# Kernel tuning notes

Hardware: AMD Instinct MI355X
Metric: run time of the kernel (lower is better)

The kernel has to match this reference:

```python
import jax, jax.numpy as jnp
import numpy as np

DIM = 384
HEADS = 8
HEAD_DIM = DIM // HEADS
TEM_LEN = 400
SCALE = HEAD_DIM ** -0.5


def setup_inputs() -> dict:
    key = jax.random.key(0)
    ks = jax.random.split(key, 12)
    B, Lq, Lkv = 16, 1024, 1424
    inp = {
        'tem_mask': jax.random.normal(ks[0], (B, TEM_LEN, DIM), jnp.float32),
        'search_mask': jax.random.normal(ks[1], (B, Lkv - TEM_LEN, DIM), jnp.float32),
        'q': jax.random.normal(ks[2], (B, Lq, DIM), jnp.float32),
        'kv': jax.random.normal(ks[3], (B, Lkv, DIM), jnp.float32),
        'attn_pos': jax.random.normal(ks[4], (1, HEADS, Lq, Lkv), jnp.float32),
        # learned params (attn_pos_encoding_only=True: q, fused kv, proj)
        'q_w': jax.random.normal(ks[5], (DIM, DIM), jnp.float32) * 0.02,
        'q_b': jnp.zeros((DIM,), jnp.float32),
        'kv_w': jax.random.normal(ks[6], (2 * DIM, DIM), jnp.float32) * 0.02,
        'kv_b': jnp.zeros((2 * DIM,), jnp.float32),
        'proj_w': jax.random.normal(ks[7], (DIM, DIM), jnp.float32) * 0.02,
        'proj_b': jnp.zeros((DIM,), jnp.float32),
    }
    return inp


def reference(tem_mask, search_mask, q, kv, attn_pos, q_w, q_b, kv_w, kv_b, proj_w, proj_b):
    B, Lq, C = q.shape
    Lkv = kv.shape[1]
    # projections
    qh = (q @ q_w.T + q_b).reshape(B, Lq, HEADS, HEAD_DIM).transpose(0, 2, 1, 3)  # (B,H,Lq,hd)
    kvp = kv @ kv_w.T + kv_b                                                      # (B,Lkv,2C)
    k = kvp[..., :C]
    v = kvp[..., C:]
    # additive masks on v before head split (template tokens first, then search)
    v = jnp.concatenate([v[:, :TEM_LEN] + tem_mask, v[:, TEM_LEN:] + search_mask], axis=1)
    kh = k.reshape(B, Lkv, HEADS, HEAD_DIM).transpose(0, 2, 1, 3)  # (B,H,Lkv,hd)
    vh = v.reshape(B, Lkv, HEADS, HEAD_DIM).transpose(0, 2, 1, 3)  # (B,H,Lkv,hd)
    # scaled scores + untied positional bias, softmax over keys
    attn = jnp.einsum('bhqd,bhkd->bhqk', qh, kh) * SCALE + attn_pos
    attn = jax.nn.softmax(attn, axis=-1)
    x = jnp.einsum('bhqk,bhkd->bhqd', attn, vh)
    x = x.transpose(0, 2, 1, 3).reshape(B, Lq, C)
    return x @ proj_w.T + proj_b
```

## Files before the change

kernel.cpp:

```cpp
#include <hip/hip_runtime.h>
#include <stdint.h>

#define NB 16
#define NH 8
#define LQ 1024
#define LKV 1424
#define LKVP 1472
#define DIMC 384
#define NKVT 23
#define TEM 400
#define QSCALE 0.20823509f
#define LOG2E_F 1.4426950408889634f

typedef __attribute__((ext_vector_type(4))) float f32x4;
typedef __attribute__((ext_vector_type(8))) short bf16x8;
typedef __attribute__((ext_vector_type(4))) unsigned short us4;
typedef __attribute__((ext_vector_type(2))) unsigned int u32x2;
typedef __attribute__((ext_vector_type(4))) unsigned int u32x4;

__device__ __forceinline__ unsigned short f2b(float f) {
  unsigned int u = __builtin_bit_cast(unsigned int, f);
  u += 0x7fffu + ((u >> 16) & 1u);
  return (unsigned short)(u >> 16);
}
__device__ __forceinline__ float b2f(unsigned short u) {
  return __builtin_bit_cast(float, (unsigned int)u << 16);
}

__device__ __forceinline__ void gload_lds16(const void* gsrc, void* ldst) {
  __builtin_amdgcn_global_load_lds(
      (const __attribute__((address_space(1))) void*)gsrc,
      (__attribute__((address_space(3))) void*)ldst, 16, 0, 0);
}

__global__ __launch_bounds__(256) void conv_swz(const float* __restrict__ in,
                                                unsigned short* __restrict__ out, int nch) {
  int i = blockIdx.x * 256 + threadIdx.x;
  if (i >= nch) return;
  int row = i / 48, ch = i - row * 48;
  const float* src = in + (size_t)row * DIMC + ch * 8;
  f32x4 x = *(const f32x4*)src;
  f32x4 y = *(const f32x4*)(src + 4);
  bf16x8 o;
  o[0] = (short)f2b(x[0]); o[1] = (short)f2b(x[1]);
  o[2] = (short)f2b(x[2]); o[3] = (short)f2b(x[3]);
  o[4] = (short)f2b(y[0]); o[5] = (short)f2b(y[1]);
  o[6] = (short)f2b(y[2]); o[7] = (short)f2b(y[3]);
  int blk = ch >> 3, c3 = (ch & 7) ^ (row & 7);
  *(bf16x8*)(out + (size_t)row * DIMC + blk * 64 + c3 * 8) = o;
}

__global__ __launch_bounds__(256) void zero_qpad(unsigned short* Qp) {
  int r = blockIdx.x * 256 + threadIdx.x;
  u32x4 z = {0u, 0u, 0u, 0u};
  *(u32x4*)(Qp + (size_t)r * 64 + 48) = z;
  *(u32x4*)(Qp + (size_t)r * 64 + 56) = z;
}
__global__ __launch_bounds__(256) void zero_kpad(unsigned short* Kp) {
  int r = blockIdx.x * 256 + threadIdx.x;
  int s = r % LKVP;
  unsigned short* row = Kp + (size_t)r * 64;
  u32x4 z = {0u, 0u, 0u, 0u};
  if (s < LKV) {
    *(u32x4*)(row + (6 ^ (s & 7)) * 8) = z;
    *(u32x4*)(row + (7 ^ (s & 7)) * 8) = z;
  } else {
#pragma unroll
    for (int c = 0; c < 64; c += 8) *(u32x4*)(row + c) = z;
  }
}
__global__ __launch_bounds__(256) void zero_vpad(unsigned short* Vt) {
  int i = blockIdx.x * 256 + threadIdx.x;
  int row = i / 6, x = 2 + i - (i / 6) * 6;
  int d = row % 48;
  u32x4 z = {0u, 0u, 0u, 0u};
  *(u32x4*)(Vt + (size_t)row * LKVP + 1408 + ((x ^ d) & 7) * 8) = z;
}

__global__ __launch_bounds__(256) void prep_pos(const float* __restrict__ pos,
                                                unsigned short* __restrict__ posb) {
  const int t = blockIdx.x, h = blockIdx.z;
  const int wave = threadIdx.x >> 6, lane = threadIdx.x & 63;
  const int q16 = blockIdx.y * 4 + wave;
  const int l16 = lane & 15, g = lane >> 4;
  const int q = q16 * 16 + l16;
  const float* pr = pos + ((size_t)h * LQ + q) * LKV;
  unsigned short vals[16];
  const unsigned short NEG = f2b(-1e30f);
#pragma unroll
  for (int ni = 0; ni < 4; ++ni) {
    if (t * 64 + ni * 16 < LKV) {
      f32x4 v = *(const f32x4*)(pr + t * 64 + ni * 16 + 4 * g);
#pragma unroll
      for (int r = 0; r < 4; ++r) vals[ni * 4 + r] = f2b(v[r] * LOG2E_F);
    } else {
#pragma unroll
      for (int r = 0; r < 4; ++r) vals[ni * 4 + r] = NEG;
    }
  }
  unsigned short* op = posb + ((((size_t)h * 64 + q16) * NKVT + t) * 64 + lane) * 16;
  bf16x8 a, b;
#pragma unroll
  for (int i = 0; i < 8; ++i) { a[i] = (short)vals[i]; b[i] = (short)vals[8 + i]; }
  *(bf16x8*)op = a;
  *(bf16x8*)(op + 8) = b;
}

template <int MODE>
__global__ __launch_bounds__(256) void proj_gemm(
    const unsigned short* __restrict__ A, const unsigned short* __restrict__ Wb,
    const float* __restrict__ bias, const float* __restrict__ tem,
    const float* __restrict__ srch, unsigned short* __restrict__ Oq,
    unsigned short* __restrict__ Ok, unsigned short* __restrict__ Ovt,
    float* __restrict__ Of) {
  __shared__ unsigned short Ash[128 * 64];
  __shared__ unsigned short Bsh[128 * 64];
  const int tid = threadIdx.x;
  const int lane = tid & 63, l16 = lane & 15, g = lane >> 4;
  const int wave = tid >> 6, wm = wave >> 1, wn = wave & 1;
  const int n0 = blockIdx.x * 128, m0 = blockIdx.y * 128;

  f32x4 acc[4][4];
#pragma unroll
  for (int i = 0; i < 4; ++i)
#pragma unroll
    for (int j = 0; j < 4; ++j) { f32x4 z = {0.f, 0.f, 0.f, 0.f}; acc[i][j] = z; }

  const char* Abase = (const char*)A + (size_t)m0 * 768;
  const char* Bbase = (const char*)Wb + (size_t)n0 * 768;

  for (int ks = 0; ks < 6; ++ks) {
    __syncthreads();
#pragma unroll
    for (int rnd = 0; rnd < 4; ++rnd) {
      int idx = tid + rnd * 256;
      int row = idx >> 3, chunk = idx & 7;
      gload_lds16(Abase + (size_t)row * 768 + ks * 128 + chunk * 16,
                  (char*)Ash + idx * 16);
    }
#pragma unroll
    for (int rnd = 0; rnd < 4; ++rnd) {
      int idx = tid + rnd * 256;
      int row = idx >> 3, chunk = idx & 7;
      gload_lds16(Bbase + (size_t)row * 768 + ks * 128 + chunk * 16,
                  (char*)Bsh + idx * 16);
    }
    asm volatile("s_waitcnt vmcnt(0)" ::: "memory");
    __syncthreads();
#pragma unroll
    for (int kk = 0; kk < 2; ++kk) {
      bf16x8 a[4], bb[4];
#pragma unroll
      for (int mi = 0; mi < 4; ++mi) {
        int row = wm * 64 + mi * 16 + l16;
        a[mi] = *(const bf16x8*)((char*)Ash + row * 128 + (((g + 4 * kk) ^ (row & 7)) << 4));
      }
#pragma unroll
      for (int ni = 0; ni < 4; ++ni) {
        int row = wn * 64 + ni * 16 + l16;
        bb[ni] = *(const bf16x8*)((char*)Bsh + row * 128 + (((g + 4 * kk) ^ (row & 7)) << 4));
      }
#pragma unroll
      for (int mi = 0; mi < 4; ++mi)
#pragma unroll
        for (int ni = 0; ni < 4; ++ni)
          acc[mi][ni] = __builtin_amdgcn_mfma_f32_16x16x32_bf16(a[mi], bb[ni], acc[mi][ni], 0, 0, 0);
    }
  }

#pragma unroll
  for (int mi = 0; mi < 4; ++mi) {
    const int m_g0 = m0 + wm * 64 + mi * 16 + 4 * g;
#pragma unroll
    for (int ni = 0; ni < 4; ++ni) {
      const int n_g = n0 + wn * 64 + ni * 16 + l16;
      const float bv = bias[n_g];
      if (MODE == 0) {
        const int hh = n_g / 48, d = n_g - hh * 48;
#pragma unroll
        for (int r = 0; r < 4; ++r) {
          const int m_g = m_g0 + r;
          const int b = m_g >> 10, m = m_g & 1023;
          Oq[(((size_t)b * NH + hh) * LQ + m) * 64 + d] = f2b((acc[mi][ni][r] + bv) * QSCALE);
        }
      } else if (MODE == 2) {
#pragma unroll
        for (int r = 0; r < 4; ++r)
          Of[(size_t)(m_g0 + r) * DIMC + n_g] = acc[mi][ni][r] + bv;
      } else {
        const int b = m_g0 / LKV, s0 = m_g0 - b * LKV;
        if (n_g < DIMC) {
          const int hh = n_g / 48, d = n_g - hh * 48;
#pragma unroll
          for (int r = 0; r < 4; ++r) {
            const int s = s0 + r;
            const int dsw = (d & 7) | ((((d >> 3) ^ (s & 7)) & 7) << 3);
            Ok[(((size_t)b * NH + hh) * LKVP + s) * 64 + dsw] = f2b(acc[mi][ni][r] + bv);
          }
        } else {
          const int c = n_g - DIMC, hh = c / 48, d = c - hh * 48;
          const float* mb = (s0 < TEM)
                                ? tem + ((size_t)b * TEM + s0) * DIMC + c
                                : srch + ((size_t)b * (LKV - TEM) + (s0 - TEM)) * DIMC + c;
          const int off = s0 & 63;
          const int soff = (s0 & ~63) | ((((off >> 3) ^ d) & 7) << 3) | (off & 7);
          us4 pk;
#pragma unroll
          for (int r = 0; r < 4; ++r)
            pk[r] = f2b(acc[mi][ni][r] + bv + mb[(size_t)r * DIMC]);
          *(us4*)(Ovt + (((size_t)b * NH + hh) * 48 + d) * LKVP + soff) = pk;
        }
      }
    }
  }
}

__device__ __forceinline__ void stage_tile(const char* kbase, const char* vbase, int t,
                                           char* kdst, char* vdst, int wave, int lane) {
  const char* ks = kbase + (size_t)t * 8192 + wave * 2048 + lane * 16;
  char* kd = kdst + wave * 2048;
  gload_lds16(ks, kd);
  gload_lds16(ks + 1024, kd + 1024);
  if (wave < 3) {
    const char* vs = vbase + (size_t)(wave * 16 + (lane >> 3)) * (LKVP * 2) +
                     (size_t)t * 128 + (lane & 7) * 16;
    char* vd = vdst + wave * 2048;
    gload_lds16(vs, vd);
    gload_lds16(vs + 8 * (LKVP * 2), vd + 1024);
  }
}

__global__ __launch_bounds__(256, 4) void attn_fwd(
    const unsigned short* __restrict__ posb, const unsigned short* __restrict__ Qp,
    const unsigned short* __restrict__ Kp, const unsigned short* __restrict__ Vt,
    unsigned short* __restrict__ X) {
  __shared__ unsigned short Ksh[2][64 * 64];
  __shared__ unsigned short Vsh[2][48 * 64];
  __shared__ unsigned short Psh[4][16 * 64];

  const int tid = threadIdx.x;
  const int lane = tid & 63, l16 = lane & 15, g = lane >> 4;
  const int wave = tid >> 6;
  const int bid = blockIdx.x;
  const int bh = bid & 127, qt = bid >> 7;
  const int b = bh >> 3, h = bh & 7;
  const int qrow = qt * 128 + wave * 32;

  bf16x8 qf[2][2];
#pragma unroll
  for (int qs = 0; qs < 2; ++qs) {
    const unsigned short* qb = Qp + ((size_t)bh * LQ + qrow + qs * 16 + l16) * 64 + 8 * g;
    qf[qs][0] = *(const bf16x8*)qb;
    qf[qs][1] = *(const bf16x8*)(qb + 32);
  }

  float m_run[2] = {-1e30f, -1e30f}, l_run[2] = {0.f, 0.f};
  f32x4 o[2][3];
#pragma unroll
  for (int qs = 0; qs < 2; ++qs)
#pragma unroll
    for (int d = 0; d < 3; ++d) { f32x4 z = {0.f, 0.f, 0.f, 0.f}; o[qs][d] = z; }

  const char* kbase = (const char*)(Kp + (size_t)bh * LKVP * 64);
  const char* vbase = (const char*)(Vt + (size_t)bh * 48 * LKVP);
  const int q16b = qt * 8 + wave * 2;
  const unsigned short* pq0 = posb + (((size_t)h * 64 + q16b) * NKVT) * 1024 + lane * 16;
  const unsigned short* pq1 = pq0 + (size_t)NKVT * 1024;
  char* pbase = (char*)&Psh[wave][0] + l16 * 128;
  const int swz = (l16 & 7) << 4;

  stage_tile(kbase, vbase, 0, (char*)&Ksh[0][0], (char*)&Vsh[0][0], wave, lane);
  asm volatile("s_waitcnt vmcnt(0)" ::: "memory");
  __syncthreads();

  int buf = 0;
  for (int t = 0; t < NKVT; ++t) {
    if (t + 1 < NKVT)
      stage_tile(kbase, vbase, t + 1, (char*)&Ksh[buf ^ 1][0], (char*)&Vsh[buf ^ 1][0],
                 wave, lane);

    bf16x8 pA0 = *(const bf16x8*)(pq0);
    bf16x8 pA1 = *(const bf16x8*)(pq0 + 8);
    bf16x8 pB0 = *(const bf16x8*)(pq1);
    bf16x8 pB1 = *(const bf16x8*)(pq1 + 8);
    pq0 += 1024; pq1 += 1024;

    f32x4 s[2][4];
#pragma unroll
    for (int qs = 0; qs < 2; ++qs)
#pragma unroll
      for (int ni = 0; ni < 4; ++ni) { f32x4 z = {0.f, 0.f, 0.f, 0.f}; s[qs][ni] = z; }
#pragma unroll
    for (int ni = 0; ni < 4; ++ni) {
      const int krow = ni * 16 + l16;
      const char* kr = (const char*)&Ksh[buf][0] + krow * 128;
      bf16x8 kf0 = *(const bf16x8*)(kr + ((g ^ (krow & 7)) << 4));
      bf16x8 kf1 = *(const bf16x8*)(kr + (((g + 4) ^ (krow & 7)) << 4));
      s[0][ni] = __builtin_amdgcn_mfma_f32_16x16x32_bf16(kf0, qf[0][0], s[0][ni], 0, 0, 0);
      s[0][ni] = __builtin_amdgcn_mfma_f32_16x16x32_bf16(kf1, qf[0][1], s[0][ni], 0, 0, 0);
      s[1][ni] = __builtin_amdgcn_mfma_f32_16x16x32_bf16(kf0, qf[1][0], s[1][ni], 0, 0, 0);
      s[1][ni] = __builtin_amdgcn_mfma_f32_16x16x32_bf16(kf1, qf[1][1], s[1][ni], 0, 0, 0);
    }

    bf16x8 af[2][2];
#pragma unroll
    for (int qs = 0; qs < 2; ++qs) {
      float x[16];
#pragma unroll
      for (int ni = 0; ni < 4; ++ni)
#pragma unroll
        for (int r = 0; r < 4; ++r) {
          const int idx = ni * 4 + r;
          unsigned short u =
              (unsigned short)(qs == 0 ? (idx < 8 ? pA0[idx] : pA1[idx - 8])
                                       : (idx < 8 ? pB0[idx] : pB1[idx - 8]));
          x[idx] = s[qs][ni][r] + b2f(u);
        }
      float mx = x[0];
#pragma unroll
      for (int i = 1; i < 16; ++i) mx = fmaxf(mx, x[i]);
      mx = fmaxf(mx, __shfl_xor(mx, 16));
      mx = fmaxf(mx, __shfl_xor(mx, 32));
      if (__any(mx > m_run[qs] + 8.f)) {
        const float mn = fmaxf(m_run[qs], mx);
        const float al = exp2f(m_run[qs] - mn);
        m_run[qs] = mn;
        l_run[qs] *= al;
#pragma unroll
        for (int r = 0; r < 4; ++r) {
          const float ab = __shfl(al, 4 * (lane >> 4) + r);
          o[qs][0][r] *= ab; o[qs][1][r] *= ab; o[qs][2][r] *= ab;
        }
      }
      const float base = m_run[qs];
      float sum = 0.f;
#pragma unroll
      for (int i = 0; i < 16; ++i) { x[i] = exp2f(x[i] - base); sum += x[i]; }
      sum += __shfl_xor(sum, 16);
      sum += __shfl_xor(sum, 32);
      l_run[qs] += sum;

#pragma unroll
      for (int ni = 0; ni < 4; ++ni) {
        unsigned int lo, hi;
        asm("v_cvt_pk_bf16_f32 %0, %1, %2" : "=v"(lo) : "v"(x[4 * ni]), "v"(x[4 * ni + 1]));
        asm("v_cvt_pk_bf16_f32 %0, %1, %2" : "=v"(hi) : "v"(x[4 * ni + 2]), "v"(x[4 * ni + 3]));
        u32x2 pk = {lo, hi};
        *(u32x2*)(pbase + ((32 * ni + 8 * g) ^ swz)) = pk;
      }
      af[qs][0] = *(const bf16x8*)(pbase + ((16 * g) ^ swz));
      af[qs][1] = *(const bf16x8*)(pbase + ((64 + 16 * g) ^ swz));
    }

#pragma unroll
    for (int dn = 0; dn < 3; ++dn) {
      const int vr = 16 * dn + l16;
      const char* vrp = (const char*)&Vsh[buf][0] + vr * 128;
      bf16x8 vf0 = *(const bf16x8*)(vrp + ((g ^ (vr & 7)) << 4));
      bf16x8 vf1 = *(const bf16x8*)(vrp + (((g + 4) ^ (vr & 7)) << 4));
      o[0][dn] = __builtin_amdgcn_mfma_f32_16x16x32_bf16(af[0][0], vf0, o[0][dn], 0, 0, 0);
      o[0][dn] = __builtin_amdgcn_mfma_f32_16x16x32_bf16(af[0][1], vf1, o[0][dn], 0, 0, 0);
      o[1][dn] = __builtin_amdgcn_mfma_f32_16x16x32_bf16(af[1][0], vf0, o[1][dn], 0, 0, 0);
      o[1][dn] = __builtin_amdgcn_mfma_f32_16x16x32_bf16(af[1][1], vf1, o[1][dn], 0, 0, 0);
    }

    asm volatile("s_waitcnt vmcnt(0)" ::: "memory");
    __syncthreads();
    buf ^= 1;
  }

#pragma unroll
  for (int qs = 0; qs < 2; ++qs) {
    const float linv = 1.f / l_run[qs];
#pragma unroll
    for (int r = 0; r < 4; ++r) {
      const float ib = __shfl(linv, 4 * (lane >> 4) + r);
      const int m = qrow + qs * 16 + 4 * g + r;
#pragma unroll
      for (int dn = 0; dn < 3; ++dn) {
        const int c = h * 48 + 16 * dn + l16;
        const int cs = (c & ~63) | (c & 7) | ((((c >> 3) & 7) ^ (m & 7)) << 3);
        X[((size_t)b * LQ + m) * DIMC + cs] = f2b(o[qs][dn][r] * ib);
      }
    }
  }
}

extern "C" void kernel_launch(void* const* d_in, const int* in_sizes, int n_in,
                              void* d_out, int out_size, void* d_ws, size_t ws_size,
                              hipStream_t stream) {
  const float* tem  = (const float*)d_in[0];
  const float* srch = (const float*)d_in[1];
  const float* q    = (const float*)d_in[2];
  const float* kv   = (const float*)d_in[3];
  const float* pos  = (const float*)d_in[4];
  const float* q_w  = (const float*)d_in[5];
  const float* q_b  = (const float*)d_in[6];
  const float* kv_w = (const float*)d_in[7];
  const float* kv_b = (const float*)d_in[8];
  const float* p_w  = (const float*)d_in[9];
  const float* p_b  = (const float*)d_in[10];
  float* out = (float*)d_out;

  char* w = (char*)d_ws;
  unsigned short* Qp   = (unsigned short*)(w);
  unsigned short* Kp   = (unsigned short*)(w + 16777216);
  unsigned short* Vt   = (unsigned short*)(w + 40894464);
  unsigned short* X    = (unsigned short*)(w + 58982400);
  unsigned short* qb   = X;
  unsigned short* posb = (unsigned short*)(w + 71565312);
  unsigned short* kvb  = (unsigned short*)(w + 95682560);
  unsigned short* qwb  = (unsigned short*)(w + 113180672);
  unsigned short* kvwb = (unsigned short*)(w + 113475584);
  unsigned short* pwb  = (unsigned short*)(w + 114065408);

  conv_swz<<<3072, 256, 0, stream>>>(q, qb, 16384 * 48);
  conv_swz<<<4272, 256, 0, stream>>>(kv, kvb, 22784 * 48);
  conv_swz<<<72, 256, 0, stream>>>(q_w, qwb, 384 * 48);
  conv_swz<<<144, 256, 0, stream>>>(kv_w, kvwb, 768 * 48);
  conv_swz<<<72, 256, 0, stream>>>(p_w, pwb, 384 * 48);
  zero_qpad<<<512, 256, 0, stream>>>(Qp);
  zero_kpad<<<736, 256, 0, stream>>>(Kp);
  zero_vpad<<<144, 256, 0, stream>>>(Vt);
  prep_pos<<<dim3(NKVT, 16, NH), 256, 0, stream>>>(pos, posb);
  proj_gemm<0><<<dim3(3, 128), 256, 0, stream>>>(qb, qwb, q_b, nullptr, nullptr,
                                                 Qp, nullptr, nullptr, nullptr);
  proj_gemm<1><<<dim3(6, 178), 256, 0, stream>>>(kvb, kvwb, kv_b, tem, srch,
                                                 nullptr, Kp, Vt, nullptr);
  attn_fwd<<<1024, 256, 0, stream>>>(posb, Qp, Kp, Vt, X);
  proj_gemm<2><<<dim3(3, 128), 256, 0, stream>>>(X, pwb, p_b, nullptr, nullptr,
                                                 nullptr, nullptr, nullptr, out);
}
```

Before: 233.0 us.

## Merge prep launches, coalesce pos prep via LDS, restructure attention softmax/PV

Merges the five conversion launches into one kernel and the three pad-zeroing launches into another, cutting launch count. prep_pos now reads contiguous 64-wide rows coalesced and transposes through shared memory before writing the bf16 layout, fixing strided global reads. In attention, the positional bias is preloaded directly as the score accumulator init (saving adds), and softmax/pack/PV for the two query subtiles are interleaved so MFMA on one overlaps VALU work on the other. This adds branching in the merged kernels and extra LDS use in prep_pos.

```diff
diff --git a/kernel.cpp b/kernel.cpp
--- a/kernel.cpp
+++ b/kernel.cpp
@@ -23,9 +23,6 @@
   u += 0x7fffu + ((u >> 16) & 1u);
   return (unsigned short)(u >> 16);
 }
-__device__ __forceinline__ float b2f(unsigned short u) {
-  return __builtin_bit_cast(float, (unsigned int)u << 16);
-}
 
 __device__ __forceinline__ void gload_lds16(const void* gsrc, void* ldst) {
   __builtin_amdgcn_global_load_lds(
@@ -33,77 +30,97 @@
       (__attribute__((address_space(3))) void*)ldst, 16, 0, 0);
 }
 
-__global__ __launch_bounds__(256) void conv_swz(const float* __restrict__ in,
-                                                unsigned short* __restrict__ out, int nch) {
+__global__ __launch_bounds__(256) void conv_all(
+    const float* __restrict__ q, const float* __restrict__ kv,
+    const float* __restrict__ qw, const float* __restrict__ kvw,
+    const float* __restrict__ pw, unsigned short* __restrict__ qb,
+    unsigned short* __restrict__ kvb, unsigned short* __restrict__ qwb,
+    unsigned short* __restrict__ kvwb, unsigned short* __restrict__ pwb) {
   int i = blockIdx.x * 256 + threadIdx.x;
-  if (i >= nch) return;
+  const float* src;
+  unsigned short* dst;
+  if (i < 16384 * 48) { src = q; dst = qb; }
+  else if (i < 39168 * 48) { i -= 16384 * 48; src = kv; dst = kvb; }
+  else if (i < 39552 * 48) { i -= 39168 * 48; src = qw; dst = qwb; }
+  else if (i < 40320 * 48) { i -= 39552 * 48; src = kvw; dst = kvwb; }
+  else if (i < 40704 * 48) { i -= 40320 * 48; src = pw; dst = pwb; }
+  else return;
   int row = i / 48, ch = i - row * 48;
-  const float* src = in + (size_t)row * DIMC + ch * 8;
-  f32x4 x = *(const f32x4*)src;
-  f32x4 y = *(const f32x4*)(src + 4);
+  const float* sp = src + (size_t)row * DIMC + ch * 8;
+  f32x4 x = *(const f32x4*)sp;
+  f32x4 y = *(const f32x4*)(sp + 4);
   bf16x8 o;
   o[0] = (short)f2b(x[0]); o[1] = (short)f2b(x[1]);
   o[2] = (short)f2b(x[2]); o[3] = (short)f2b(x[3]);
   o[4] = (short)f2b(y[0]); o[5] = (short)f2b(y[1]);
   o[6] = (short)f2b(y[2]); o[7] = (short)f2b(y[3]);
   int blk = ch >> 3, c3 = (ch & 7) ^ (row & 7);
-  *(bf16x8*)(out + (size_t)row * DIMC + blk * 64 + c3 * 8) = o;
-}
-
-__global__ __launch_bounds__(256) void zero_qpad(unsigned short* Qp) {
-  int r = blockIdx.x * 256 + threadIdx.x;
+  *(bf16x8*)(dst + (size_t)row * DIMC + blk * 64 + c3 * 8) = o;
+}
+
+__global__ __launch_bounds__(256) void zero_pads(unsigned short* Qp, unsigned short* Kp,
+                                                 unsigned short* Vt) {
+  int i = blockIdx.x * 256 + threadIdx.x;
   u32x4 z = {0u, 0u, 0u, 0u};
-  *(u32x4*)(Qp + (size_t)r * 64 + 48) = z;
-  *(u32x4*)(Qp + (size_t)r * 64 + 56) = z;
-}
-__global__ __launch_bounds__(256) void zero_kpad(unsigned short* Kp) {
-  int r = blockIdx.x * 256 + threadIdx.x;
-  int s = r % LKVP;
-  unsigned short* row = Kp + (size_t)r * 64;
-  u32x4 z = {0u, 0u, 0u, 0u};
-  if (s < LKV) {
-    *(u32x4*)(row + (6 ^ (s & 7)) * 8) = z;
-    *(u32x4*)(row + (7 ^ (s & 7)) * 8) = z;
-  } else {
-#pragma unroll
-    for (int c = 0; c < 64; c += 8) *(u32x4*)(row + c) = z;
-  }
-}
-__global__ __launch_bounds__(256) void zero_vpad(unsigned short* Vt) {
-  int i = blockIdx.x * 256 + threadIdx.x;
-  int row = i / 6, x = 2 + i - (i / 6) * 6;
-  int d = row % 48;
-  u32x4 z = {0u, 0u, 0u, 0u};
-  *(u32x4*)(Vt + (size_t)row * LKVP + 1408 + ((x ^ d) & 7) * 8) = z;
+  if (i < 131072) {
+    *(u32x4*)(Qp + (size_t)i * 64 + 48) = z;
+    *(u32x4*)(Qp + (size_t)i * 64 + 56) = z;
+  } else if (i < 131072 + 188416) {
+    int r = i - 131072;
+    int s = r % LKVP;
+    unsigned short* row = Kp + (size_t)r * 64;
+    if (s < LKV) {
+      *(u32x4*)(row + (6 ^ (s & 7)) * 8) = z;
+      *(u32x4*)(row + (7 ^ (s & 7)) * 8) = z;
+    } else {
+#pragma unroll
+      for (int c = 0; c < 64; c += 8) *(u32x4*)(row + c) = z;
+    }
+  } else if (i < 131072 + 188416 + 36864) {
+    int j = i - 319488;
+    int row = j / 6, x = 2 + j - (j / 6) * 6;
+    int d = row % 48;
+    *(u32x4*)(Vt + (size_t)row * LKVP + 1408 + ((x ^ d) & 7) * 8) = z;
+  }
 }
 
 __global__ __launch_bounds__(256) void prep_pos(const float* __restrict__ pos,
                                                 unsigned short* __restrict__ posb) {
-  const int t = blockIdx.x, h = blockIdx.z;
+  __shared__ float lds[4][1024];
   const int wave = threadIdx.x >> 6, lane = threadIdx.x & 63;
-  const int q16 = blockIdx.y * 4 + wave;
   const int l16 = lane & 15, g = lane >> 4;
-  const int q = q16 * 16 + l16;
-  const float* pr = pos + ((size_t)h * LQ + q) * LKV;
-  unsigned short vals[16];
-  const unsigned short NEG = f2b(-1e30f);
-#pragma unroll
-  for (int ni = 0; ni < 4; ++ni) {
-    if (t * 64 + ni * 16 < LKV) {
-      f32x4 v = *(const f32x4*)(pr + t * 64 + ni * 16 + 4 * g);
-#pragma unroll
-      for (int r = 0; r < 4; ++r) vals[ni * 4 + r] = f2b(v[r] * LOG2E_F);
-    } else {
-#pragma unroll
-      for (int r = 0; r < 4; ++r) vals[ni * 4 + r] = NEG;
-    }
-  }
-  unsigned short* op = posb + ((((size_t)h * 64 + q16) * NKVT + t) * 64 + lane) * 16;
-  bf16x8 a, b;
-#pragma unroll
-  for (int i = 0; i < 8; ++i) { a[i] = (short)vals[i]; b[i] = (short)vals[8 + i]; }
-  *(bf16x8*)op = a;
-  *(bf16x8*)(op + 8) = b;
+  const int q16 = blockIdx.x, h = blockIdx.y;
+  float* L = &lds[wave][0];
+
+  for (int t = wave; t < NKVT; t += 4) {
+#pragma unroll
+    for (int i = 0; i < 4; ++i) {
+      const int row = i * 4 + g;
+      const int gcol = t * 64 + l16 * 4;
+      f32x4 v;
+      if (gcol < LKV) {
+        v = *(const f32x4*)(pos + ((size_t)h * LQ + q16 * 16 + row) * LKV + gcol);
+        v *= LOG2E_F;
+      } else {
+        f32x4 neg = {-1e30f, -1e30f, -1e30f, -1e30f};
+        v = neg;
+      }
+      *(f32x4*)(L + row * 64 + ((l16 ^ (row & 7)) << 2)) = v;
+    }
+    unsigned short vals[16];
+#pragma unroll
+    for (int ni = 0; ni < 4; ++ni) {
+      f32x4 wv = *(const f32x4*)(L + l16 * 64 + (((4 * ni + g) ^ (l16 & 7)) << 2));
+#pragma unroll
+      for (int r = 0; r < 4; ++r) vals[4 * ni + r] = f2b(wv[r]);
+    }
+    unsigned short* op = posb + ((((size_t)h * 64 + q16) * NKVT + t) * 64 + lane) * 16;
+    bf16x8 a, b;
+#pragma unroll
+    for (int k = 0; k < 8; ++k) { a[k] = (short)vals[k]; b[k] = (short)vals[8 + k]; }
+    *(bf16x8*)op = a;
+    *(bf16x8*)(op + 8) = b;
+  }
 }
 
 template <int MODE>
@@ -230,6 +247,57 @@
   }
 }
 
+__device__ __forceinline__ void softmax16(f32x4 (&sx)[4], float& m_run, float& l_run,
+                                          f32x4& o0, f32x4& o1, f32x4& o2, int lane) {
+  float a0 = fmaxf(fmaxf(sx[0][0], sx[0][1]), sx[0][2]);
+  float a1 = fmaxf(fmaxf(sx[0][3], sx[1][0]), sx[1][1]);
+  float a2 = fmaxf(fmaxf(sx[1][2], sx[1][3]), sx[2][0]);
+  float a3 = fmaxf(fmaxf(sx[2][1], sx[2][2]), sx[2][3]);
+  float a4 = fmaxf(fmaxf(sx[3][0], sx[3][1]), sx[3][2]);
+  float mx = fmaxf(fmaxf(fmaxf(a0, a1), fmaxf(a2, a3)), fmaxf(a4, sx[3][3]));
+  mx = fmaxf(mx, __shfl_xor(mx, 16));
+  mx = fmaxf(mx, __shfl_xor(mx, 32));
+  if (__any(mx > m_run + 8.f)) {
+    const float mn = fmaxf(m_run, mx);
+    const float al = exp2f(m_run - mn);
+    m_run = mn;
+    l_run *= al;
+#pragma unroll
+    for (int r = 0; r < 4; ++r) {
+      const float ab = __shfl(al, 4 * (lane >> 4) + r);
+      o0[r] *= ab; o1[r] *= ab; o2[r] *= ab;
+    }
+  }
+  const float base = m_run;
+#pragma unroll
+  for (int ni = 0; ni < 4; ++ni)
+#pragma unroll
+    for (int r = 0; r < 4; ++r) sx[ni][r] = exp2f(sx[ni][r] - base);
+  float s0 = (sx[0][0] + sx[0][1]) + (sx[0][2] + sx[0][3]);
+  float s1 = (sx[1][0] + sx[1][1]) + (sx[1][2] + sx[1][3]);
+  float s2 = (sx[2][0] + sx[2][1]) + (sx[2][2] + sx[2][3]);
+  float s3 = (sx[3][0] + sx[3][1]) + (sx[3][2] + sx[3][3]);
+  float sum = (s0 + s1) + (s2 + s3);
+  sum += __shfl_xor(sum, 16);
+  sum += __shfl_xor(sum, 32);
+  l_run += sum;
+}
+
+__device__ __forceinline__ void packP(const f32x4 (&sx)[4], char* pbase, int swz, int g,
+                                      bf16x8& af0, bf16x8& af1) {
+#pragma unroll
+  for (int ni = 0; ni < 4; ++ni) {
+    float e0 = sx[ni][0], e1 = sx[ni][1], e2 = sx[ni][2], e3 = sx[ni][3];
+    unsigned int lo, hi;
+    asm("v_cvt_pk_bf16_f32 %0, %1, %2" : "=v"(lo) : "v"(e0), "v"(e1));
+    asm("v_cvt_pk_bf16_f32 %0, %1, %2" : "=v"(hi) : "v"(e2), "v"(e3));
+    u32x2 pk = {lo, hi};
+    *(u32x2*)(pbase + ((32 * ni + 8 * g) ^ swz)) = pk;
+  }
+  af0 = *(const bf16x8*)(pbase + ((16 * g) ^ swz));
+  af1 = *(const bf16x8*)(pbase + ((64 + 16 * g) ^ swz));
+}
+
 __global__ __launch_bounds__(256, 4) void attn_fwd(
     const unsigned short* __restrict__ posb, const unsigned short* __restrict__ Qp,
     const unsigned short* __restrict__ Kp, const unsigned short* __restrict__ Vt,
@@ -254,7 +322,7 @@
     qf[qs][1] = *(const bf16x8*)(qb + 32);
   }
 
-  float m_run[2] = {-1e30f, -1e30f}, l_run[2] = {0.f, 0.f};
+  float m_run0 = -1e30f, m_run1 = -1e30f, l_run0 = 0.f, l_run1 = 0.f;
   f32x4 o[2][3];
 #pragma unroll
   for (int qs = 0; qs < 2; ++qs)
@@ -279,89 +347,61 @@
       stage_tile(kbase, vbase, t + 1, (char*)&Ksh[buf ^ 1][0], (char*)&Vsh[buf ^ 1][0],
                  wave, lane);
 
-    bf16x8 pA0 = *(const bf16x8*)(pq0);
-    bf16x8 pA1 = *(const bf16x8*)(pq0 + 8);
-    bf16x8 pB0 = *(const bf16x8*)(pq1);
-    bf16x8 pB1 = *(const bf16x8*)(pq1 + 8);
+    u32x4 w0 = *(const u32x4*)(pq0);
+    u32x4 w1 = *(const u32x4*)(pq0 + 8);
+    u32x4 w2 = *(const u32x4*)(pq1);
+    u32x4 w3 = *(const u32x4*)(pq1 + 8);
     pq0 += 1024; pq1 += 1024;
 
-    f32x4 s[2][4];
-#pragma unroll
-    for (int qs = 0; qs < 2; ++qs)
-#pragma unroll
-      for (int ni = 0; ni < 4; ++ni) { f32x4 z = {0.f, 0.f, 0.f, 0.f}; s[qs][ni] = z; }
+    f32x4 s0[4], s1[4];
+#pragma unroll
+    for (int k = 0; k < 4; ++k) {
+      const int ni = k >> 1, j2 = (k & 1) * 2;
+      unsigned int a = w0[k], bb_ = w1[k], c = w2[k], d = w3[k];
+      s0[ni][j2]     = __builtin_bit_cast(float, a << 16);
+      s0[ni][j2 + 1] = __builtin_bit_cast(float, a & 0xffff0000u);
+      s0[ni + 2][j2]     = __builtin_bit_cast(float, bb_ << 16);
+      s0[ni + 2][j2 + 1] = __builtin_bit_cast(float, bb_ & 0xffff0000u);
+      s1[ni][j2]     = __builtin_bit_cast(float, c << 16);
+      s1[ni][j2 + 1] = __builtin_bit_cast(float, c & 0xffff0000u);
+      s1[ni + 2][j2]     = __builtin_bit_cast(float, d << 16);
+      s1[ni + 2][j2 + 1] = __builtin_bit_cast(float, d & 0xffff0000u);
+    }
+
 #pragma unroll
     for (int ni = 0; ni < 4; ++ni) {
       const int krow = ni * 16 + l16;
       const char* kr = (const char*)&Ksh[buf][0] + krow * 128;
       bf16x8 kf0 = *(const bf16x8*)(kr + ((g ^ (krow & 7)) << 4));
       bf16x8 kf1 = *(const bf16x8*)(kr + (((g + 4) ^ (krow & 7)) << 4));
-      s[0][ni] = __builtin_amdgcn_mfma_f32_16x16x32_bf16(kf0, qf[0][0], s[0][ni], 0, 0, 0);
-      s[0][ni] = __builtin_amdgcn_mfma_f32_16x16x32_bf16(kf1, qf[0][1], s[0][ni], 0, 0, 0);
-      s[1][ni] = __builtin_amdgcn_mfma_f32_16x16x32_bf16(kf0, qf[1][0], s[1][ni], 0, 0, 0);
-      s[1][ni] = __builtin_amdgcn_mfma_f32_16x16x32_bf16(kf1, qf[1][1], s[1][ni], 0, 0, 0);
-    }
-
-    bf16x8 af[2][2];
-#pragma unroll
-    for (int qs = 0; qs < 2; ++qs) {
-      float x[16];
-#pragma unroll
-      for (int ni = 0; ni < 4; ++ni)
-#pragma unroll
-        for (int r = 0; r < 4; ++r) {
-          const int idx = ni * 4 + r;
-          unsigned short u =
-              (unsigned short)(qs == 0 ? (idx < 8 ? pA0[idx] : pA1[idx - 8])
-                                       : (idx < 8 ? pB0[idx] : pB1[idx - 8]));
-          x[idx] = s[qs][ni][r] + b2f(u);
-        }
-      float mx = x[0];
-#pragma unroll
-      for (int i = 1; i < 16; ++i) mx = fmaxf(mx, x[i]);
-      mx = fmaxf(mx, __shfl_xor(mx, 16));
-      mx = fmaxf(mx, __shfl_xor(mx, 32));
-      if (__any(mx > m_run[qs] + 8.f)) {
-        const float mn = fmaxf(m_run[qs], mx);
-        const float al = exp2f(m_run[qs] - mn);
-        m_run[qs] = mn;
-        l_run[qs] *= al;
-#pragma unroll
-        for (int r = 0; r < 4; ++r) {
-          const float ab = __shfl(al, 4 * (lane >> 4) + r);
-          o[qs][0][r] *= ab; o[qs][1][r] *= ab; o[qs][2][r] *= ab;
-        }
-      }
-      const float base = m_run[qs];
-      float sum = 0.f;
-#pragma unroll
-      for (int i = 0; i < 16; ++i) { x[i] = exp2f(x[i] - base); sum += x[i]; }
-      sum += __shfl_xor(sum, 16);
-      sum += __shfl_xor(sum, 32);
-      l_run[qs] += sum;
-
-#pragma unroll
-      for (int ni = 0; ni < 4; ++ni) {
-        unsigned int lo, hi;
-        asm("v_cvt_pk_bf16_f32 %0, %1, %2" : "=v"(lo) : "v"(x[4 * ni]), "v"(x[4 * ni + 1]));
-        asm("v_cvt_pk_bf16_f32 %0, %1, %2" : "=v"(hi) : "v"(x[4 * ni + 2]), "v"(x[4 * ni + 3]));
-        u32x2 pk = {lo, hi};
-        *(u32x2*)(pbase + ((32 * ni + 8 * g) ^ swz)) = pk;
-      }
-      af[qs][0] = *(const bf16x8*)(pbase + ((16 * g) ^ swz));
-      af[qs][1] = *(const bf16x8*)(pbase + ((64 + 16 * g) ^ swz));
-    }
-
+      s0[ni] = __builtin_amdgcn_mfma_f32_16x16x32_bf16(kf0, qf[0][0], s0[ni], 0, 0, 0);
+      s0[ni] = __builtin_amdgcn_mfma_f32_16x16x32_bf16(kf1, qf[0][1], s0[ni], 0, 0, 0);
+      s1[ni] = __builtin_amdgcn_mfma_f32_16x16x32_bf16(kf0, qf[1][0], s1[ni], 0, 0, 0);
+      s1[ni] = __builtin_amdgcn_mfma_f32_16x16x32_bf16(kf1, qf[1][1], s1[ni], 0, 0, 0);
+    }
+
+    softmax16(s0, m_run0, l_run0, o[0][0], o[0][1], o[0][2], lane);
+    bf16x8 af00, af01, af10, af11;
+    packP(s0, pbase, swz, g, af00, af01);
+    softmax16(s1, m_run1, l_run1, o[1][0], o[1][1], o[1][2], lane);
 #pragma unroll
     for (int dn = 0; dn < 3; ++dn) {
       const int vr = 16 * dn + l16;
       const char* vrp = (const char*)&Vsh[buf][0] + vr * 128;
       bf16x8 vf0 = *(const bf16x8*)(vrp + ((g ^ (vr & 7)) << 4));
       bf16x8 vf1 = *(const bf16x8*)(vrp + (((g + 4) ^ (vr & 7)) << 4));
-      o[0][dn] = __builtin_amdgcn_mfma_f32_16x16x32_bf16(af[0][0], vf0, o[0][dn], 0, 0, 0);
-      o[0][dn] = __builtin_amdgcn_mfma_f32_16x16x32_bf16(af[0][1], vf1, o[0][dn], 0, 0, 0);
-      o[1][dn] = __builtin_amdgcn_mfma_f32_16x16x32_bf16(af[1][0], vf0, o[1][dn], 0, 0, 0);
-      o[1][dn] = __builtin_amdgcn_mfma_f32_16x16x32_bf16(af[1][1], vf1, o[1][dn], 0, 0, 0);
+      o[0][dn] = __builtin_amdgcn_mfma_f32_16x16x32_bf16(af00, vf0, o[0][dn], 0, 0, 0);
+      o[0][dn] = __builtin_amdgcn_mfma_f32_16x16x32_bf16(af01, vf1, o[0][dn], 0, 0, 0);
+    }
+    packP(s1, pbase, swz, g, af10, af11);
+#pragma unroll
+    for (int dn = 0; dn < 3; ++dn) {
+      const int vr = 16 * dn + l16;
+      const char* vrp = (const char*)&Vsh[buf][0] + vr * 128;
+      bf16x8 vf0 = *(const bf16x8*)(vrp + ((g ^ (vr & 7)) << 4));
+      bf16x8 vf1 = *(const bf16x8*)(vrp + (((g + 4) ^ (vr & 7)) << 4));
+      o[1][dn] = __builtin_amdgcn_mfma_f32_16x16x32_bf16(af10, vf0, o[1][dn], 0, 0, 0);
+      o[1][dn] = __builtin_amdgcn_mfma_f32_16x16x32_bf16(af11, vf1, o[1][dn], 0, 0, 0);
     }
 
     asm volatile("s_waitcnt vmcnt(0)" ::: "memory");
@@ -371,7 +411,7 @@
 
 #pragma unroll
   for (int qs = 0; qs < 2; ++qs) {
-    const float linv = 1.f / l_run[qs];
+    const float linv = 1.f / (qs == 0 ? l_run0 : l_run1);
 #pragma unroll
     for (int r = 0; r < 4; ++r) {
       const float ib = __shfl(linv, 4 * (lane >> 4) + r);
@@ -414,15 +454,9 @@
   unsigned short* kvwb = (unsigned short*)(w + 113475584);
   unsigned short* pwb  = (unsigned short*)(w + 114065408);
 
-  conv_swz<<<3072, 256, 0, stream>>>(q, qb, 16384 * 48);
-  conv_swz<<<4272, 256, 0, stream>>>(kv, kvb, 22784 * 48);
-  conv_swz<<<72, 256, 0, stream>>>(q_w, qwb, 384 * 48);
-  conv_swz<<<144, 256, 0, stream>>>(kv_w, kvwb, 768 * 48);
-  conv_swz<<<72, 256, 0, stream>>>(p_w, pwb, 384 * 48);
-  zero_qpad<<<512, 256, 0, stream>>>(Qp);
-  zero_kpad<<<736, 256, 0, stream>>>(Kp);
-  zero_vpad<<<144, 256, 0, stream>>>(Vt);
-  prep_pos<<<dim3(NKVT, 16, NH), 256, 0, stream>>>(pos, posb);
+  conv_all<<<7632, 256, 0, stream>>>(q, kv, q_w, kv_w, p_w, qb, kvb, qwb, kvwb, pwb);
+  zero_pads<<<1392, 256, 0, stream>>>(Qp, Kp, Vt);
+  prep_pos<<<dim3(64, 8), 256, 0, stream>>>(pos, posb);
   proj_gemm<0><<<dim3(3, 128), 256, 0, stream>>>(qb, qwb, q_b, nullptr, nullptr,
                                                  Qp, nullptr, nullptr, nullptr);
   proj_gemm<1><<<dim3(6, 178), 256, 0, stream>>>(kvb, kvwb, kv_b, tem, srch,
```

Result: faster. 214.4 us (-8.0%).
